# Performance work log

Hardware: AMD Instinct MI355X
Metric: run time of the kernel (lower is better)

The kernel has to match this reference:

```python
import jax, jax.numpy as jnp
import numpy as np

D = 512       # hidden_size (attention defaults hardcode 512)
N = 8         # num_heads
H = D // N    # depth per head = 64
FF = 2048     # FFN filter size (hardcoded)
EPS = 1e-6


def _layer_norm(x, gamma, beta):
    # matches functional layer_norm: biased variance, eps inside sqrt
    mean = jnp.mean(x, axis=-1, keepdims=True)
    var = jnp.mean((x - mean) ** 2, axis=-1, keepdims=True)
    return gamma * ((x - mean) / jnp.sqrt(var + EPS)) + beta


def setup_inputs() -> dict:
    key = jax.random.key(0)
    ks = jax.random.split(key, 12)
    B, S = 8, 1024
    s = lambda k, shape, scale: jax.random.normal(k, shape, jnp.float32) * scale
    return {
        "inputs": s(ks[0], (B, S, D), 1.0),
        "attention_bias": jnp.zeros((B, 1, 1, S), jnp.float32),
        "ln1_g": jnp.ones((D,), jnp.float32),
        "ln1_b": jnp.zeros((D,), jnp.float32),
        "wq": s(ks[1], (D, N, H), D ** -0.5),
        "wk": s(ks[2], (D, N, H), D ** -0.5),
        "wv": s(ks[3], (D, N, H), D ** -0.5),
        "wo": s(ks[4], (N, H, D), D ** -0.5),
        "ln2_g": jnp.ones((D,), jnp.float32),
        "ln2_b": jnp.zeros((D,), jnp.float32),
        "w1": s(ks[5], (D, FF), D ** -0.5),
        "b1": jnp.zeros((FF,), jnp.float32),
        "w2": s(ks[6], (FF, D), FF ** -0.5),
        "b2": jnp.zeros((D,), jnp.float32),
    }


def reference(inputs, attention_bias, ln1_g, ln1_b, wq, wk, wv, wo,
              ln2_g, ln2_b, w1, b1, w2, b2):
    # --- self-attention block (pre-LN, residual) ---
    y = _layer_norm(inputs, ln1_g, ln1_b)
    q = jnp.einsum('bsd,dnh->bsnh', y, wq) * (H ** -0.5)
    k = jnp.einsum('bsd,dnh->bsnh', y, wk)
    v = jnp.einsum('bsd,dnh->bsnh', y, wv)
    # logits[b,n,f,t] = sum_h k[b,t,n,h] * q[b,f,n,h]
    logits = jnp.einsum('btnh,bfnh->bnft', k, q) + attention_bias
    weights = jax.nn.softmax(logits, axis=3)
    attn = jnp.einsum('bnft,btnh->bfnh', weights, v)
    attn_out = jnp.einsum('bfnh,nhd->bfd', attn, wo)
    x = inputs + attn_out

    # --- FFN block (pre-LN, residual) ---
    y2 = _layer_norm(x, ln2_g, ln2_b)
    h = jax.nn.relu(jnp.einsum('bsd,df->bsf', y2, w1) + b1)
    ffn_out = jnp.einsum('bsf,fd->bsd', h, w2) + b2
    return x + ffn_out
```

## Files before the change

### kernel.cpp

```cpp
#include <hip/hip_runtime.h>
#include <stdint.h>

typedef unsigned short u16;
typedef __attribute__((ext_vector_type(8))) __bf16 bf16x8;
typedef __attribute__((ext_vector_type(4))) float f32x4;

__device__ __forceinline__ float bf2f(u16 u) {
    union { unsigned int i; float f; } c; c.i = ((unsigned int)u) << 16; return c.f;
}
__device__ __forceinline__ u16 f2bf(float f) {
    union { float f; unsigned int i; } c; c.f = f;
    unsigned int u = c.i;
    u += 0x7FFFu + ((u >> 16) & 1u);
    return (u16)(u >> 16);
}
__device__ __forceinline__ bool sniff_f32(const unsigned* probe) {
    return probe && ((*probe & 0xFFFFu) == 0u);
}
__device__ __forceinline__ float lde(const void* p, size_t i, bool isf32) {
    return isf32 ? ((const float*)p)[i] : bf2f(((const u16*)p)[i]);
}
__device__ __forceinline__ void g2lds16(const void* g, void* l) {
    __builtin_amdgcn_global_load_lds(
        (__attribute__((address_space(1))) void*)(uintptr_t)g,
        (__attribute__((address_space(3))) void*)(unsigned int)(uintptr_t)l,
        16, 0, 0);
}

__global__ void prep_weights(const void* __restrict__ wq, const void* __restrict__ wk,
                             const void* __restrict__ wv, const void* __restrict__ wo,
                             const void* __restrict__ w1, const void* __restrict__ w2,
                             u16* __restrict__ wqkvT, u16* __restrict__ woT,
                             u16* __restrict__ w1T, u16* __restrict__ w2T,
                             const unsigned* probe) {
    __shared__ u16 t[32][33];
    const bool isf32 = sniff_f32(probe);
    const int id = blockIdx.x;
    const void* src; u16* dst; int R, C, cb, rb; float scale = 1.f;
    if (id < 1024) {
        const int which = id >> 8, tl = id & 255;
        R = 512; C = 512; cb = (tl & 15) * 32; rb = (tl >> 4) * 32;
        if (which == 0)      { src = wq; dst = wqkvT;              scale = 0.125f; }
        else if (which == 1) { src = wk; dst = wqkvT + 512 * 512; }
        else if (which == 2) { src = wv; dst = wqkvT + 1024 * 512; }
        else                 { src = wo; dst = woT; }
    } else if (id < 2048) {
        const int tl = id - 1024; src = w1; dst = w1T; R = 512; C = 2048;
        cb = (tl & 63) * 32; rb = (tl >> 6) * 32;
    } else {
        const int tl = id - 2048; src = w2; dst = w2T; R = 2048; C = 512;
        cb = (tl & 15) * 32; rb = (tl >> 4) * 32;
    }
    const int tx = threadIdx.x, ty = threadIdx.y;
#pragma unroll
    for (int i = 0; i < 4; i++)
        t[ty + i * 8][tx] = f2bf(lde(src, (size_t)(rb + ty + i * 8) * C + cb + tx, isf32));
    __syncthreads();
#pragma unroll
    for (int i = 0; i < 4; i++) {
        float v = bf2f(t[tx][ty + i * 8]) * scale;
        dst[(size_t)(cb + ty + i * 8) * R + rb + tx] = f2bf(v);
    }
}

__global__ __launch_bounds__(256) void ln_any(const void* __restrict__ x,
                                              const void* __restrict__ gw,
                                              const void* __restrict__ bw,
                                              u16* __restrict__ y,
                                              const unsigned* probe_x,
                                              const unsigned* probe_gb) {
    const bool xf32 = sniff_f32(probe_x);
    const bool gf32 = sniff_f32(probe_gb);
    const int lane = threadIdx.x & 63, wave = threadIdx.x >> 6;
    const int r = blockIdx.x * 4 + wave;
    union U8 { uint4 v; u16 s[8]; };
    float xs[8];
    if (xf32) {
        const float4* xr = (const float4*)((const float*)x + (size_t)r * 512 + lane * 8);
        float4 p0 = xr[0], p1 = xr[1];
        xs[0]=p0.x; xs[1]=p0.y; xs[2]=p0.z; xs[3]=p0.w;
        xs[4]=p1.x; xs[5]=p1.y; xs[6]=p1.z; xs[7]=p1.w;
    } else {
        U8 xu; xu.v = *(const uint4*)((const u16*)x + (size_t)r * 512 + lane * 8);
#pragma unroll
        for (int j = 0; j < 8; j++) xs[j] = bf2f(xu.s[j]);
    }
    float s1 = 0.f, s2 = 0.f;
#pragma unroll
    for (int j = 0; j < 8; j++) { s1 += xs[j]; s2 += xs[j] * xs[j]; }
#pragma unroll
    for (int d = 1; d < 64; d <<= 1) { s1 += __shfl_xor(s1, d); s2 += __shfl_xor(s2, d); }
    const float mean = s1 * (1.f / 512.f);
    const float var = s2 * (1.f / 512.f) - mean * mean;
    const float rstd = rsqrtf(var + 1e-6f);
    float gs[8], bs[8];
    if (gf32) {
        const float4* gr = (const float4*)((const float*)gw + lane * 8);
        const float4* br = (const float4*)((const float*)bw + lane * 8);
        float4 g0 = gr[0], g1 = gr[1], b0 = br[0], b1 = br[1];
        gs[0]=g0.x; gs[1]=g0.y; gs[2]=g0.z; gs[3]=g0.w; gs[4]=g1.x; gs[5]=g1.y; gs[6]=g1.z; gs[7]=g1.w;
        bs[0]=b0.x; bs[1]=b0.y; bs[2]=b0.z; bs[3]=b0.w; bs[4]=b1.x; bs[5]=b1.y; bs[6]=b1.z; bs[7]=b1.w;
    } else {
        U8 gu; gu.v = *(const uint4*)((const u16*)gw + lane * 8);
        U8 bu; bu.v = *(const uint4*)((const u16*)bw + lane * 8);
#pragma unroll
        for (int j = 0; j < 8; j++) { gs[j] = bf2f(gu.s[j]); bs[j] = bf2f(bu.s[j]); }
    }
    union U8 ou;
#pragma unroll
    for (int j = 0; j < 8; j++)
        ou.s[j] = f2bf(gs[j] * ((xs[j] - mean) * rstd) + bs[j]);
    *(uint4*)(y + (size_t)r * 512 + lane * 8) = ou.v;
}

template <int EPI, int TM>
__global__ __launch_bounds__(256, 2) void gemm_bt(const u16* __restrict__ A,
                                                  const u16* __restrict__ Bt,
                                                  const void* __restrict__ bias,
                                                  const void* __restrict__ res,
                                                  void* __restrict__ out,
                                                  u16* __restrict__ out2,
                                                  const unsigned* probe,
                                                  int M, int N, int K) {
    constexpr int ACH = TM / 16;
    constexpr int MI = TM / 32;
    __shared__ __align__(16) u16 lA[2][TM * 32];
    __shared__ __align__(16) u16 lB[2][128 * 32];
    const int tid = threadIdx.x, wave = tid >> 6, lane = tid & 63;
    const int m0 = blockIdx.x * TM, n0 = blockIdx.y * 128;
    const int wm = (wave >> 1) * (TM / 2), wn = (wave & 1) * 64;
    const int row = lane & 15, quad = lane >> 4;
    f32x4 acc[MI][4];
#pragma unroll
    for (int i = 0; i < MI; i++)
#pragma unroll
        for (int j = 0; j < 4; j++) acc[i][j] = (f32x4){0.f, 0.f, 0.f, 0.f};
    const u16* Ab = A + (size_t)m0 * K;
    const u16* Bb = Bt + (size_t)n0 * K;

    auto stage = [&](int buf, int k0) {
#pragma unroll
        for (int c = 0; c < (ACH + 8 + 3) / 4; c++) {
            const int ch = c * 4 + wave;
            if (ch < ACH) {
                const int e = ch * 64 + lane;
                const int r = e >> 2, col = (e & 3) * 8;
                g2lds16(Ab + (size_t)r * K + k0 + col, (char*)lA[buf] + ch * 1024);
            } else if (ch < ACH + 8) {
                const int c2 = ch - ACH;
                const int e = c2 * 64 + lane;
                const int r = e >> 2, col = (e & 3) * 8;
                g2lds16(Bb + (size_t)r * K + k0 + col, (char*)lB[buf] + c2 * 1024);
            }
        }
    };

    stage(0, 0);
    int cur = 0;
    for (int k0 = 0; k0 < K; k0 += 32) {
        __syncthreads();
        if (k0 + 32 < K) stage(cur ^ 1, k0 + 32);
        bf16x8 af[MI], bfr[4];
#pragma unroll
        for (int t = 0; t < MI; t++)
            af[t]  = *(const bf16x8*)(lA[cur] + (wm + t * 16 + row) * 32 + quad * 8);
#pragma unroll
        for (int t = 0; t < 4; t++)
            bfr[t] = *(const bf16x8*)(lB[cur] + (wn + t * 16 + row) * 32 + quad * 8);
#pragma unroll
        for (int i = 0; i < MI; i++)
#pragma unroll
            for (int j = 0; j < 4; j++)
                acc[i][j] = __builtin_amdgcn_mfma_f32_16x16x32_bf16(af[i], bfr[j], acc[i][j], 0, 0, 0);
        cur ^= 1;
    }
    const bool isf32 = sniff_f32(probe);
#pragma unroll
    for (int i = 0; i < MI; i++) {
        const int gm = m0 + wm + i * 16 + quad * 4;
#pragma unroll
        for (int j = 0; j < 4; j++) {
            const int gn = n0 + wn + j * 16 + row;
            float bv = 0.f;
            if (EPI == 2 || EPI == 3) bv = lde(bias, gn, isf32);
#pragma unroll
            for (int r = 0; r < 4; r++) {
                float v = acc[i][j][r];
                const int gmr = gm + r;
                size_t idx = (size_t)gmr * N + gn;
                if (EPI == 1) {
                    ((u16*)out)[idx] = f2bf(v + lde(res, idx, isf32));
                } else if (EPI == 2) {
                    v += bv;
                    ((u16*)out)[idx] = f2bf(v > 0.f ? v : 0.f);
                } else if (EPI == 3) {
                    v += bv + bf2f(((const u16*)res)[idx]);
                    if (isf32) ((float*)out)[idx] = v;
                    else       ((u16*)out)[idx] = f2bf(v);
                } else {
                    if (gn < 1024) {
                        ((u16*)out)[(size_t)gmr * 1024 + gn] = f2bf(v);
                    } else {
                        const int j2 = gn - 1024, n = j2 >> 6, h2 = j2 & 63;
                        const int b = gmr >> 10, t = gmr & 1023;
                        out2[(((size_t)b * 8 + n) * 64 + h2) * 1024 + t] = f2bf(v);
                    }
                }
            }
        }
    }
}

__global__ __launch_bounds__(256, 2) void attn_fused(const u16* __restrict__ qk,
                                                     const u16* __restrict__ vT,
                                                     const void* __restrict__ biasp,
                                                     u16* __restrict__ attn,
                                                     const unsigned* probe) {
    __shared__ __align__(16) u16 lQ[64 * 64];
    __shared__ __align__(16) u16 lK[128 * 64];
    __shared__ __align__(16) u16 lV[64 * 128];
    const bool isf32 = sniff_f32(probe);
    const int tid = threadIdx.x, wave = tid >> 6, lane = tid & 63;
    const int row = lane & 15, quad = lane >> 4;
    const int bn = blockIdx.x, b = bn >> 3, n = bn & 7;
    const int f0 = blockIdx.y * 64;
    const u16* Qg = qk + (size_t)(b * 1024 + f0) * 1024 + n * 64;
    const u16* Kg = qk + (size_t)(b * 1024) * 1024 + 512 + n * 64;
    const u16* Vg = vT + (size_t)bn * 65536;

#pragma unroll
    for (int j = 0; j < 2; j++) {
        const int ch = wave * 2 + j, e = ch * 64 + lane;
        const int rq = e >> 3, cq = ((e & 7) ^ (rq & 7)) * 8;
        g2lds16(Qg + (size_t)rq * 1024 + cq, (char*)lQ + ch * 1024);
    }
    float m_i = -1e30f, l_i = 0.f;
    f32x4 oacc[4];
#pragma unroll
    for (int h = 0; h < 4; h++) oacc[h] = (f32x4){0.f, 0.f, 0.f, 0.f};

    for (int t0 = 0; t0 < 1024; t0 += 128) {
        __syncthreads();
#pragma unroll
        for (int j = 0; j < 4; j++) {
            const int ch = wave * 4 + j, e = ch * 64 + lane;
            const int rk = e >> 3, ck = ((e & 7) ^ (rk & 7)) * 8;
            g2lds16(Kg + (size_t)(t0 + rk) * 1024 + ck, (char*)lK + ch * 1024);
            const int rv = e >> 4, cv = ((e & 15) ^ (rv & 7)) * 8;
            g2lds16(Vg + (size_t)rv * 1024 + t0 + cv, (char*)lV + ch * 1024);
        }
        __syncthreads();
        f32x4 s[8];
#pragma unroll
        for (int nt = 0; nt < 8; nt++) s[nt] = (f32x4){0.f, 0.f, 0.f, 0.f};
        const int fr = wave * 16 + row;
        bf16x8 bq[2];
#pragma unroll
        for (int ks = 0; ks < 2; ks++)
            bq[ks] = *(const bf16x8*)(lQ + fr * 64 + (((ks * 4 + quad) ^ (fr & 7)) * 8));
#pragma unroll
        for (int nt = 0; nt < 8; nt++) {
            const int tr = nt * 16 + row;
#pragma unroll
            for (int ks = 0; ks < 2; ks++) {
                bf16x8 ak = *(const bf16x8*)(lK + tr * 64 + (((ks * 4 + quad) ^ (tr & 7)) * 8));
                s[nt] = __builtin_amdgcn_mfma_f32_16x16x32_bf16(ak, bq[ks], s[nt], 0, 0, 0);
            }
        }
        float mx = -1e30f;
#pragma unroll
        for (int nt = 0; nt < 8; nt++) {
            const size_t bidx = (size_t)b * 1024 + t0 + nt * 16 + quad * 4;
            float bv4[4];
            if (isf32) {
                float4 t4 = *(const float4*)((const float*)biasp + bidx);
                bv4[0] = t4.x; bv4[1] = t4.y; bv4[2] = t4.z; bv4[3] = t4.w;
            } else {
                union { uint2 v; u16 s[4]; } bu;
                bu.v = *(const uint2*)((const u16*)biasp + bidx);
#pragma unroll
                for (int r = 0; r < 4; r++) bv4[r] = bf2f(bu.s[r]);
            }
#pragma unroll
            for (int r = 0; r < 4; r++) {
                s[nt][r] += bv4[r];
                mx = fmaxf(mx, s[nt][r]);
            }
        }
        mx = fmaxf(mx, __shfl_xor(mx, 16));
        mx = fmaxf(mx, __shfl_xor(mx, 32));
        const float mn = fmaxf(m_i, mx);
        const float alpha = __expf(m_i - mn);
        float rs = 0.f;
#pragma unroll
        for (int nt = 0; nt < 8; nt++)
#pragma unroll
            for (int r = 0; r < 4; r++) {
                float p = __expf(s[nt][r] - mn);
                s[nt][r] = p;
                rs += p;
            }
        rs += __shfl_xor(rs, 16);
        rs += __shfl_xor(rs, 32);
        l_i = l_i * alpha + rs;
        m_i = mn;
#pragma unroll
        for (int h = 0; h < 4; h++)
#pragma unroll
            for (int r = 0; r < 4; r++) oacc[h][r] *= alpha;
#pragma unroll
        for (int ks = 0; ks < 4; ks++) {
            unsigned pw[4];
#pragma unroll
            for (int g = 0; g < 2; g++) {
                pw[g * 2 + 0] = (unsigned)f2bf(s[ks * 2 + g][0]) | ((unsigned)f2bf(s[ks * 2 + g][1]) << 16);
                pw[g * 2 + 1] = (unsigned)f2bf(s[ks * 2 + g][2]) | ((unsigned)f2bf(s[ks * 2 + g][3]) << 16);
            }
            union { unsigned u[4]; bf16x8 v8; } bb;
#pragma unroll
            for (int w = 0; w < 4; w++) {
                const int srcl = ((((quad & 1) << 1) | (w >> 1)) << 4) | row;
                const unsigned lo = (unsigned)__shfl((int)pw[(w & 1)], srcl);
                const unsigned hi = (unsigned)__shfl((int)pw[2 + (w & 1)], srcl);
                bb.u[w] = (quad & 2) ? hi : lo;
            }
#pragma unroll
            for (int ht = 0; ht < 4; ht++) {
                const int vr = ht * 16 + row;
                bf16x8 av = *(const bf16x8*)(lV + vr * 128 + (((ks * 4 + quad) ^ (vr & 7)) * 8));
                oacc[ht] = __builtin_amdgcn_mfma_f32_16x16x32_bf16(av, bb.v8, oacc[ht], 0, 0, 0);
            }
        }
    }
    const float inv = 1.f / l_i;
    const int f = f0 + wave * 16 + row;
#pragma unroll
    for (int ht = 0; ht < 4; ht++) {
        uint2 ov;
        ov.x = (unsigned)f2bf(oacc[ht][0] * inv) | ((unsigned)f2bf(oacc[ht][1] * inv) << 16);
        ov.y = (unsigned)f2bf(oacc[ht][2] * inv) | ((unsigned)f2bf(oacc[ht][3] * inv) << 16);
        *(uint2*)(attn + (size_t)(b * 1024 + f) * 512 + n * 64 + ht * 16 + quad * 4) = ov;
    }
}

extern "C" void kernel_launch(void* const* d_in, const int* in_sizes, int n_in,
                              void* d_out, int out_size, void* d_ws, size_t ws_size,
                              hipStream_t stream) {
    const void* inp  = d_in[0];
    const void* ab   = d_in[1];
    const void* ln1g = d_in[2];
    const void* ln1b = d_in[3];
    const void* wq   = d_in[4];
    const void* wk   = d_in[5];
    const void* wv   = d_in[6];
    const void* wo   = d_in[7];
    const void* ln2g = d_in[8];
    const void* ln2b = d_in[9];
    const void* w1   = d_in[10];
    const void* b1   = d_in[11];
    const void* w2   = d_in[12];
    const void* b2   = d_in[13];
    const unsigned* probe = (const unsigned*)d_in[2];

    char* ws = (char*)d_ws;
    size_t off = 0;
    auto alloc = [&](size_t bytes) -> void* { void* p = ws + off; off += bytes; return p; };
    u16* wqkvT = (u16*)alloc(1536 * 512 * 2);
    u16* woT   = (u16*)alloc(512 * 512 * 2);
    u16* w1T   = (u16*)alloc(2048 * 512 * 2);
    u16* w2T   = (u16*)alloc(512 * 2048 * 2);
    u16* ybuf  = (u16*)alloc((size_t)8192 * 512 * 2);
    u16* qk    = (u16*)alloc((size_t)8192 * 1024 * 2);
    u16* vT    = (u16*)alloc((size_t)64 * 64 * 1024 * 2);
    u16* attn  = (u16*)alloc((size_t)8192 * 512 * 2);
    u16* xbf   = (u16*)alloc((size_t)8192 * 512 * 2);
    u16* hbuf  = qk;

    prep_weights<<<3072, dim3(32, 8), 0, stream>>>(wq, wk, wv, wo, w1, w2,
                                                   wqkvT, woT, w1T, w2T, probe);
    ln_any<<<2048, 256, 0, stream>>>(inp, ln1g, ln1b, ybuf, probe, probe);
    gemm_bt<4, 128><<<dim3(64, 12), 256, 0, stream>>>(ybuf, wqkvT, nullptr, nullptr, qk, vT, nullptr, 8192, 1536, 512);
    attn_fused<<<dim3(64, 16), 256, 0, stream>>>(qk, vT, ab, attn, probe);
    gemm_bt<1, 64><<<dim3(128, 4), 256, 0, stream>>>(attn, woT, nullptr, inp, xbf, nullptr, probe, 8192, 512, 512);
    ln_any<<<2048, 256, 0, stream>>>(xbf, ln2g, ln2b, ybuf, nullptr, probe);
    gemm_bt<2, 128><<<dim3(64, 16), 256, 0, stream>>>(ybuf, w1T, b1, nullptr, hbuf, nullptr, probe, 8192, 2048, 512);
    gemm_bt<3, 64><<<dim3(128, 4), 256, 0, stream>>>(hbuf, w2T, b2, xbf, (u16*)d_out, nullptr, probe, 8192, 512, 2048);
}
```

Baseline: 258.9 us.

## Double-buffer K/V tiles in attention and use packed hardware bf16 conversion

The attention kernel now keeps two LDS buffers for the K and V tiles. It issues the next tile's global-to-LDS loads before computing on the current tile, and drops the second barrier per iteration, so load latency can overlap with MFMA and softmax work. Float-to-bf16 conversions in the layernorm, attention P packing and attention output now use the packed cvt_pk_bf16_f32 builtin when it is available, replacing the software rounding. LDS use in the attention kernel roughly doubles, which may limit occupancy. In-order vmcnt waits on the bias loads could also stall on the prefetches.

New measurement: 267.7 us. +3.4%, slower.

```diff
diff --git a/kernel.cpp b/kernel.cpp
--- a/kernel.cpp
+++ b/kernel.cpp
@@ -3,16 +3,33 @@
 
 typedef unsigned short u16;
 typedef __attribute__((ext_vector_type(8))) __bf16 bf16x8;
+typedef __attribute__((ext_vector_type(2))) __bf16 bf16x2;
 typedef __attribute__((ext_vector_type(4))) float f32x4;
 
 __device__ __forceinline__ float bf2f(u16 u) {
     union { unsigned int i; float f; } c; c.i = ((unsigned int)u) << 16; return c.f;
 }
-__device__ __forceinline__ u16 f2bf(float f) {
+__device__ __forceinline__ u16 f2bf_sw(float f) {
     union { float f; unsigned int i; } c; c.f = f;
     unsigned int u = c.i;
     u += 0x7FFFu + ((u >> 16) & 1u);
     return (u16)(u >> 16);
+}
+__device__ __forceinline__ unsigned f2bf2(float lo, float hi) {
+#if __has_builtin(__builtin_amdgcn_cvt_pk_bf16_f32)
+    union { bf16x2 v; unsigned u; } c;
+    c.v = __builtin_amdgcn_cvt_pk_bf16_f32(lo, hi);
+    return c.u;
+#else
+    return (unsigned)f2bf_sw(lo) | ((unsigned)f2bf_sw(hi) << 16);
+#endif
+}
+__device__ __forceinline__ u16 f2bf(float f) {
+#if __has_builtin(__builtin_amdgcn_cvt_pk_bf16_f32)
+    return (u16)(f2bf2(f, 0.f) & 0xFFFFu);
+#else
+    return f2bf_sw(f);
+#endif
 }
 __device__ __forceinline__ bool sniff_f32(const unsigned* probe) {
     return probe && ((*probe & 0xFFFFu) == 0u);
@@ -106,11 +123,13 @@
 #pragma unroll
         for (int j = 0; j < 8; j++) { gs[j] = bf2f(gu.s[j]); bs[j] = bf2f(bu.s[j]); }
     }
-    union U8 ou;
-#pragma unroll
-    for (int j = 0; j < 8; j++)
-        ou.s[j] = f2bf(gs[j] * ((xs[j] - mean) * rstd) + bs[j]);
-    *(uint4*)(y + (size_t)r * 512 + lane * 8) = ou.v;
+    uint4 ov;
+    float o[8];
+#pragma unroll
+    for (int j = 0; j < 8; j++) o[j] = gs[j] * ((xs[j] - mean) * rstd) + bs[j];
+    ov.x = f2bf2(o[0], o[1]); ov.y = f2bf2(o[2], o[3]);
+    ov.z = f2bf2(o[4], o[5]); ov.w = f2bf2(o[6], o[7]);
+    *(uint4*)(y + (size_t)r * 512 + lane * 8) = ov;
 }
 
 template <int EPI, int TM>
@@ -217,8 +236,8 @@
                                                      u16* __restrict__ attn,
                                                      const unsigned* probe) {
     __shared__ __align__(16) u16 lQ[64 * 64];
-    __shared__ __align__(16) u16 lK[128 * 64];
-    __shared__ __align__(16) u16 lV[64 * 128];
+    __shared__ __align__(16) u16 lK[2][128 * 64];
+    __shared__ __align__(16) u16 lV[2][64 * 128];
     const bool isf32 = sniff_f32(probe);
     const int tid = threadIdx.x, wave = tid >> 6, lane = tid & 63;
     const int row = lane & 15, quad = lane >> 4;
@@ -228,28 +247,36 @@
     const u16* Kg = qk + (size_t)(b * 1024) * 1024 + 512 + n * 64;
     const u16* Vg = vT + (size_t)bn * 65536;
 
+    auto stageKV = [&](int buf, int t0) {
+#pragma unroll
+        for (int j = 0; j < 4; j++) {
+            const int ch = wave * 4 + j, e = ch * 64 + lane;
+            const int rk = e >> 3, ck = ((e & 7) ^ (rk & 7)) * 8;
+            g2lds16(Kg + (size_t)(t0 + rk) * 1024 + ck, (char*)lK[buf] + ch * 1024);
+            const int rv = e >> 4, cv = ((e & 15) ^ (rv & 7)) * 8;
+            g2lds16(Vg + (size_t)rv * 1024 + t0 + cv, (char*)lV[buf] + ch * 1024);
+        }
+    };
+
 #pragma unroll
     for (int j = 0; j < 2; j++) {
         const int ch = wave * 2 + j, e = ch * 64 + lane;
         const int rq = e >> 3, cq = ((e & 7) ^ (rq & 7)) * 8;
         g2lds16(Qg + (size_t)rq * 1024 + cq, (char*)lQ + ch * 1024);
     }
+    stageKV(0, 0);
+
     float m_i = -1e30f, l_i = 0.f;
     f32x4 oacc[4];
 #pragma unroll
     for (int h = 0; h < 4; h++) oacc[h] = (f32x4){0.f, 0.f, 0.f, 0.f};
 
+    int cur = 0;
     for (int t0 = 0; t0 < 1024; t0 += 128) {
         __syncthreads();
-#pragma unroll
-        for (int j = 0; j < 4; j++) {
-            const int ch = wave * 4 + j, e = ch * 64 + lane;
-            const int rk = e >> 3, ck = ((e & 7) ^ (rk & 7)) * 8;
-            g2lds16(Kg + (size_t)(t0 + rk) * 1024 + ck, (char*)lK + ch * 1024);
-            const int rv = e >> 4, cv = ((e & 15) ^ (rv & 7)) * 8;
-            g2lds16(Vg + (size_t)rv * 1024 + t0 + cv, (char*)lV + ch * 1024);
-        }
-        __syncthreads();
+        if (t0 + 128 < 1024) stageKV(cur ^ 1, t0 + 128);
+        const u16* lKc = lK[cur];
+        const u16* lVc = lV[cur];
         f32x4 s[8];
 #pragma unroll
         for (int nt = 0; nt < 8; nt++) s[nt] = (f32x4){0.f, 0.f, 0.f, 0.f};
@@ -263,7 +290,7 @@
             const int tr = nt * 16 + row;
 #pragma unroll
             for (int ks = 0; ks < 2; ks++) {
-                bf16x8 ak = *(const bf16x8*)(lK + tr * 64 + (((ks * 4 + quad) ^ (tr & 7)) * 8));
+                bf16x8 ak = *(const bf16x8*)(lKc + tr * 64 + (((ks * 4 + quad) ^ (tr & 7)) * 8));
                 s[nt] = __builtin_amdgcn_mfma_f32_16x16x32_bf16(ak, bq[ks], s[nt], 0, 0, 0);
             }
         }
@@ -313,8 +340,8 @@
             unsigned pw[4];
 #pragma unroll
             for (int g = 0; g < 2; g++) {
-                pw[g * 2 + 0] = (unsigned)f2bf(s[ks * 2 + g][0]) | ((unsigned)f2bf(s[ks * 2 + g][1]) << 16);
-                pw[g * 2 + 1] = (unsigned)f2bf(s[ks * 2 + g][2]) | ((unsigned)f2bf(s[ks * 2 + g][3]) << 16);
+                pw[g * 2 + 0] = f2bf2(s[ks * 2 + g][0], s[ks * 2 + g][1]);
+                pw[g * 2 + 1] = f2bf2(s[ks * 2 + g][2], s[ks * 2 + g][3]);
             }
             union { unsigned u[4]; bf16x8 v8; } bb;
 #pragma unroll
@@ -327,18 +354,19 @@
 #pragma unroll
             for (int ht = 0; ht < 4; ht++) {
                 const int vr = ht * 16 + row;
-                bf16x8 av = *(const bf16x8*)(lV + vr * 128 + (((ks * 4 + quad) ^ (vr & 7)) * 8));
+                bf16x8 av = *(const bf16x8*)(lVc + vr * 128 + (((ks * 4 + quad) ^ (vr & 7)) * 8));
                 oacc[ht] = __builtin_amdgcn_mfma_f32_16x16x32_bf16(av, bb.v8, oacc[ht], 0, 0, 0);
             }
         }
+        cur ^= 1;
     }
     const float inv = 1.f / l_i;
     const int f = f0 + wave * 16 + row;
 #pragma unroll
     for (int ht = 0; ht < 4; ht++) {
         uint2 ov;
-        ov.x = (unsigned)f2bf(oacc[ht][0] * inv) | ((unsigned)f2bf(oacc[ht][1] * inv) << 16);
-        ov.y = (unsigned)f2bf(oacc[ht][2] * inv) | ((unsigned)f2bf(oacc[ht][3] * inv) << 16);
+        ov.x = f2bf2(oacc[ht][0] * inv, oacc[ht][1] * inv);
+        ov.y = f2bf2(oacc[ht][2] * inv, oacc[ht][3] * inv);
         *(uint2*)(attn + (size_t)(b * 1024 + f) * 512 + n * 64 + ht * 16 + quad * 4) = ov;
     }
 }
```
